# Performance work log

Hardware: AMD Instinct MI355X
Metric: run time of the kernel (lower is better)

The kernel has to match this reference:

```python
import jax, jax.numpy as jnp
import numpy as np

N, D = 65536, 1024  # points, in_dim == out_dim (required by the module's double use of linear.weight)


def setup_inputs() -> dict:
    key = jax.random.key(0)
    k_x, k_w, k_W, k_noise = jax.random.split(key, 4)
    x = jax.random.normal(k_x, (N, D), dtype=jnp.float32)
    w = jax.random.normal(k_w, (D,), dtype=jnp.float32)  # style vector (len == in_dim)
    # learned params of nn.Linear(in_dim, out_dim)
    W = jax.random.normal(k_W, (D, D), dtype=jnp.float32) * 0.02  # [out_dim, in_dim]
    b = jnp.zeros((D,), dtype=jnp.float32)
    # noise path: torch does randn(1, out_dim) * noise_strength each forward;
    # we materialize the raw noise deterministically for reproducibility.
    noise_strength = jnp.full((1,), 0.1, dtype=jnp.float32)
    noise_raw = jax.random.normal(k_noise, (1, D), dtype=jnp.float32)
    return {"x": x, "w": w, "W": W, "b": b,
            "noise_strength": noise_strength, "noise_raw": noise_raw}


def reference(x, w, W, b, noise_strength, noise_raw):
    # 1) plain linear: x1 = x @ W.T + b            [N, D]
    x1 = x @ W.T + b
    # 2) modulated_linear(x1, W, styles=w, noise, demodulate=True)
    #    demod coefficients: rsqrt(sum_j (W[o,j]*w[j])^2 + 1e-8)   [D]
    dcoefs = jax.lax.rsqrt(jnp.sum(jnp.square(W * w[None, :]), axis=1) + 1e-8)
    #    modulate input, dense matmul with raw weight
    x2 = (x1 * w) @ W.T                            # [N, D]
    #    fma: x2 * dcoefs + noise
    noise = noise_raw * noise_strength             # [1, D]
    x3 = x2 * dcoefs[None, :] + noise
    # 3) bias add + leaky_relu (torch default negative_slope=0.01)
    return jax.nn.leaky_relu(x3 + b, negative_slope=0.01)
```

## Files before the change

kernel.cpp:

```cpp
#include <hip/hip_runtime.h>
#include <hip/hip_bf16.h>

using bf16 = __hip_bfloat16;
typedef __attribute__((ext_vector_type(8))) short bf16x8;
typedef __attribute__((ext_vector_type(4))) float f32x4;

#define DDIM 1024

__device__ __forceinline__ void gload16(const bf16* g, bf16* l) {
    __builtin_amdgcn_global_load_lds(
        (const __attribute__((address_space(1))) void*)g,
        (__attribute__((address_space(3))) void*)l, 16, 0, 0);
}
__device__ __forceinline__ short f2b(float f) {
    return (short)__bfloat16_as_ushort(__float2bfloat16(f));
}


__global__ void prep_kernel(const float* __restrict__ W, const float* __restrict__ w,
                            const float* __restrict__ b, const float* __restrict__ nstr,
                            const float* __restrict__ nraw,
                            float* __restrict__ dco, float* __restrict__ add,
                            bf16* __restrict__ Qb) {
    int o = blockIdx.x;
    int lane = threadIdx.x;
    const float* Wrow = W + (size_t)o * DDIM;
    bf16* Qrow = Qb + (size_t)o * DDIM;
    float s = 0.f, c = 0.f;
    for (int j = lane; j < DDIM; j += 64) {
        float q = Wrow[j] * w[j];
        Qrow[j] = __float2bfloat16(q);
        s += q * q;
        c += b[j] * q;
    }
#pragma unroll
    for (int off = 32; off; off >>= 1) {
        s += __shfl_down(s, off);
        c += __shfl_down(c, off);
    }
    if (lane == 0) {
        float d = rsqrtf(s + 1e-8f);
        dco[o] = d;
        add[o] = c * d + nraw[o] * nstr[0] + b[o];
    }
}

__global__ void transpose_kernel(const float* __restrict__ W, bf16* __restrict__ Wt) {
    __shared__ bf16 tile[64][72];
    int bi = blockIdx.x * 64;
    int bj = blockIdx.y * 64;
    int r  = threadIdx.x >> 2;
    int c4 = (threadIdx.x & 3) * 16;
    const float* src = W + (size_t)(bi + r) * DDIM + bj + c4;
#pragma unroll
    for (int i = 0; i < 16; ++i) tile[r][c4 + i] = __float2bfloat16(src[i]);
    __syncthreads();
    bf16* dst = Wt + (size_t)(bj + r) * DDIM + bi + c4;
#pragma unroll
    for (int i = 0; i < 16; ++i) dst[i] = tile[c4 + i][r];
}

__global__ __launch_bounds__(256) void mgemm(const bf16* __restrict__ A,
                                             const bf16* __restrict__ B,
                                             bf16* __restrict__ C) {
    __shared__ bf16 lA[128 * 32];
    __shared__ bf16 lB[128 * 32];
    int tid  = threadIdx.x;
    int lane = tid & 63, wid = tid >> 6;
    int wr = wid >> 1, wc = wid & 1;
    int brow = blockIdx.x >> 3;
    int bcol = blockIdx.x & 7;
    const bf16* Ab = A + (size_t)brow * 128 * DDIM;
    const bf16* Bb = B + (size_t)bcol * 128 * DDIM;
    int srow = tid >> 2;
    int scol = (tid & 3) * 8;
    f32x4 acc[4][4];
#pragma unroll
    for (int m = 0; m < 4; ++m)
#pragma unroll
        for (int n = 0; n < 4; ++n) acc[m][n] = (f32x4){0.f, 0.f, 0.f, 0.f};
    int r16 = lane & 15, kh = lane >> 4;
    for (int k0 = 0; k0 < DDIM; k0 += 32) {
        gload16(Ab + (size_t)srow * DDIM + k0 + scol,        lA + tid * 8);
        gload16(Ab + (size_t)(srow + 64) * DDIM + k0 + scol, lA + (tid + 256) * 8);
        gload16(Bb + (size_t)srow * DDIM + k0 + scol,        lB + tid * 8);
        gload16(Bb + (size_t)(srow + 64) * DDIM + k0 + scol, lB + (tid + 256) * 8);
        __syncthreads();
        bf16x8 aF[4], bF[4];
#pragma unroll
        for (int m = 0; m < 4; ++m) {
            aF[m] = *(const bf16x8*)(lA + ((wr * 64 + m * 16 + r16) * 32 + kh * 8));
            bF[m] = *(const bf16x8*)(lB + ((wc * 64 + m * 16 + r16) * 32 + kh * 8));
        }
#pragma unroll
        for (int m = 0; m < 4; ++m)
#pragma unroll
            for (int n = 0; n < 4; ++n)
                acc[m][n] = __builtin_amdgcn_mfma_f32_16x16x32_bf16(aF[m], bF[n], acc[m][n], 0, 0, 0);
        __syncthreads();
    }
    int cb = lane & 15;
    int rb = (lane >> 4) * 4;
#pragma unroll
    for (int n = 0; n < 4; ++n) {
        int col = bcol * 128 + wc * 64 + n * 16 + cb;
#pragma unroll
        for (int m = 0; m < 4; ++m)
#pragma unroll
            for (int j = 0; j < 4; ++j) {
                int row = wr * 64 + m * 16 + rb + j;
                C[((size_t)brow * 128 + row) * DDIM + col] = __float2bfloat16(acc[m][n][j]);
            }
    }
}

#define BAR()  __builtin_amdgcn_s_barrier()
#define VMW(n) asm volatile("s_waitcnt vmcnt(" #n ")")
#define LGW()  asm volatile("s_waitcnt lgkmcnt(0)")

__global__ __launch_bounds__(512, 4) void big_gemm(
    const float* __restrict__ Af, const bf16* __restrict__ Bw,
    const float* __restrict__ dco, const float* __restrict__ add,
    float* __restrict__ Cf)
{
    __shared__ bf16 sA[2][256 * 32];
    __shared__ bf16 sB[2][128 * 32];

    const int tid  = threadIdx.x;
    const int lane = tid & 63;
    const int wid  = tid >> 6;
    const int wr   = wid >> 1, wc = wid & 1;
    const int r16  = lane & 15, kh = lane >> 4;
    const int fso  = (kh ^ ((r16 >> 1) & 3)) * 8;

    int bx  = blockIdx.x;
    int swz = (bx & 7) * 256 + (bx >> 3);
    int brow = swz >> 3, bcol = swz & 7;

    const float* Asrc_f = Af + (size_t)(brow * 256) * DDIM;
    const bf16*  Bsrc   = Bw + (size_t)(bcol * 128) * DDIM;

    const int sr  = tid >> 2;
    const int ssl = (tid & 3) ^ ((sr >> 1) & 3);

    f32x4 acc[4][4];
#pragma unroll
    for (int m = 0; m < 4; ++m)
#pragma unroll
        for (int n = 0; n < 4; ++n) acc[m][n] = (f32x4){0.f, 0.f, 0.f, 0.f};

    bf16x8 aF[4], bF[4];
    float4 gA0, gA1, gA2, gA3;

#define STAGE_B(buf, kt) do { \
    const bf16* _s = Bsrc + (size_t)sr * DDIM + ((kt) * 32 + ssl * 8); \
    gload16(_s, &sB[buf][tid * 8]); \
} while (0)

#define LOAD_A_F(kt) do { \
    const float* _p = Asrc_f + (size_t)sr * DDIM + ((kt) * 32 + (tid & 3) * 8); \
    gA0 = ((const float4*)_p)[0]; gA1 = ((const float4*)_p)[1]; \
    const float* _q = _p + 128 * DDIM; \
    gA2 = ((const float4*)_q)[0]; gA3 = ((const float4*)_q)[1]; \
} while (0)

#define WRITE_A(buf) do { \
    bf16x8 _pk; \
    _pk[0]=f2b(gA0.x); _pk[1]=f2b(gA0.y); _pk[2]=f2b(gA0.z); _pk[3]=f2b(gA0.w); \
    _pk[4]=f2b(gA1.x); _pk[5]=f2b(gA1.y); _pk[6]=f2b(gA1.z); _pk[7]=f2b(gA1.w); \
    *(bf16x8*)&sA[buf][sr * 32 + ssl * 8] = _pk; \
    _pk[0]=f2b(gA2.x); _pk[1]=f2b(gA2.y); _pk[2]=f2b(gA2.z); _pk[3]=f2b(gA2.w); \
    _pk[4]=f2b(gA3.x); _pk[5]=f2b(gA3.y); _pk[6]=f2b(gA3.z); _pk[7]=f2b(gA3.w); \
    *(bf16x8*)&sA[buf][(sr + 128) * 32 + ssl * 8] = _pk; \
} while (0)

#define RD_A(buf) do { \
    _Pragma("unroll") for (int _m = 0; _m < 4; ++_m) \
        aF[_m] = *(const bf16x8*)&sA[buf][(wr * 64 + _m * 16 + r16) * 32 + fso]; \
} while (0)

#define RD_B(buf) do { \
    _Pragma("unroll") for (int _n = 0; _n < 4; ++_n) \
        bF[_n] = *(const bf16x8*)&sB[buf][(wc * 64 + _n * 16 + r16) * 32 + fso]; \
} while (0)

#define MFMA16() do { \
    __builtin_amdgcn_s_setprio(1); \
    _Pragma("unroll") for (int _m = 0; _m < 4; ++_m) { \
        acc[_m][0] = __builtin_amdgcn_mfma_f32_16x16x32_bf16(aF[_m], bF[0], acc[_m][0], 0, 0, 0); \
        acc[_m][1] = __builtin_amdgcn_mfma_f32_16x16x32_bf16(aF[_m], bF[1], acc[_m][1], 0, 0, 0); \
        acc[_m][2] = __builtin_amdgcn_mfma_f32_16x16x32_bf16(aF[_m], bF[2], acc[_m][2], 0, 0, 0); \
        acc[_m][3] = __builtin_amdgcn_mfma_f32_16x16x32_bf16(aF[_m], bF[3], acc[_m][3], 0, 0, 0); \
    } \
    __builtin_amdgcn_s_setprio(0); \
} while (0)

    LOAD_A_F(0);
    STAGE_B(0, 0);
    VMW(1);
    WRITE_A(0);
    LOAD_A_F(1);
    LGW();
    VMW(4);
    BAR();

    for (int t = 0; t < 32; ++t) {
        int cur = t & 1, nxt = cur ^ 1;
        int t1 = t + 1; if (t1 > 31) t1 = 31;
        int t2 = t + 2; if (t2 > 31) t2 = 31;

        RD_A(cur); RD_B(cur);
        STAGE_B(nxt, t1);
        VMW(1);
        WRITE_A(nxt);
        LOAD_A_F(t2);
        LGW();
        BAR();
        MFMA16();
        VMW(4);
        BAR();
    }

    int cb = lane & 15;
    int rb = (lane >> 4) * 4;
#pragma unroll
    for (int n = 0; n < 4; ++n) {
        int col = bcol * 128 + wc * 64 + n * 16 + cb;
        float cm = dco[col], ca = add[col];
#pragma unroll
        for (int m = 0; m < 4; ++m) {
#pragma unroll
            for (int j = 0; j < 4; ++j) {
                int row = brow * 256 + wr * 64 + m * 16 + rb + j;
                float v = acc[m][n][j] * cm + ca;
                v = (v >= 0.f) ? v : 0.01f * v;
                Cf[(size_t)row * DDIM + col] = v;
            }
        }
    }
#undef STAGE_B
#undef LOAD_A_F
#undef WRITE_A
#undef RD_A
#undef RD_B
#undef MFMA16
}

extern "C" void kernel_launch(void* const* d_in, const int* in_sizes, int n_in,
                              void* d_out, int out_size, void* d_ws, size_t ws_size,
                              hipStream_t stream) {
    const float* x  = (const float*)d_in[0];
    const float* w  = (const float*)d_in[1];
    const float* W  = (const float*)d_in[2];
    const float* b  = (const float*)d_in[3];
    const float* ns = (const float*)d_in[4];
    const float* nr = (const float*)d_in[5];
    float* out = (float*)d_out;

    float* dco = (float*)d_ws;
    float* add = dco + DDIM;
    bf16*  Qb  = (bf16*)((char*)d_ws + 8192);
    bf16*  Wt  = (bf16*)((char*)d_ws + 8192 + 2097152);
    bf16*  Mt  = (bf16*)((char*)d_ws + 8192 + 2 * 2097152);

    int M = in_sizes[0] / DDIM;
    int grid = (M / 256) * (DDIM / 128);

    prep_kernel<<<DDIM, 64, 0, stream>>>(W, w, b, ns, nr, dco, add, Qb);
    transpose_kernel<<<dim3(16, 16), 256, 0, stream>>>(W, Wt);
    mgemm<<<64, 256, 0, stream>>>(Qb, Wt, Mt);
    big_gemm<<<grid, 512, 0, stream>>>(x, Mt, dco, add, out);
}
```

Before: 298.1 us.

## Load A fragments directly from global into registers, shrink block tile to 128x128

The big GEMM no longer stages the fp32 A operand through LDS. Each wave loads its own rows straight from global memory into registers and converts them to bf16 fragments, one k-step ahead. The block shrinks from 512 threads with a 256x128 tile to 256 threads with a 128x128 tile, so the grid doubles and each B tile is now fetched by twice as many blocks. The pipeline is reordered to prefetch B two stages ahead with one barrier per iteration, which removes the LDS writes and the second barrier but gives uncoalesced strided global A loads and more register pressure.

```diff
diff --git a/kernel.cpp b/kernel.cpp
--- a/kernel.cpp
+++ b/kernel.cpp
@@ -118,12 +118,11 @@
 #define VMW(n) asm volatile("s_waitcnt vmcnt(" #n ")")
 #define LGW()  asm volatile("s_waitcnt lgkmcnt(0)")
 
-__global__ __launch_bounds__(512, 4) void big_gemm(
+__global__ __launch_bounds__(256, 3) void big_gemm(
     const float* __restrict__ Af, const bf16* __restrict__ Bw,
     const float* __restrict__ dco, const float* __restrict__ add,
     float* __restrict__ Cf)
 {
-    __shared__ bf16 sA[2][256 * 32];
     __shared__ bf16 sB[2][128 * 32];
 
     const int tid  = threadIdx.x;
@@ -134,11 +133,11 @@
     const int fso  = (kh ^ ((r16 >> 1) & 3)) * 8;
 
     int bx  = blockIdx.x;
-    int swz = (bx & 7) * 256 + (bx >> 3);
+    int swz = (bx & 7) * 512 + (bx >> 3);
     int brow = swz >> 3, bcol = swz & 7;
 
-    const float* Asrc_f = Af + (size_t)(brow * 256) * DDIM;
-    const bf16*  Bsrc   = Bw + (size_t)(bcol * 128) * DDIM;
+    const float* Arow = Af + (size_t)(brow * 128 + wr * 64 + r16) * DDIM + kh * 8;
+    const bf16*  Bsrc = Bw + (size_t)(bcol * 128) * DDIM;
 
     const int sr  = tid >> 2;
     const int ssl = (tid & 3) ^ ((sr >> 1) & 3);
@@ -149,34 +148,30 @@
 #pragma unroll
         for (int n = 0; n < 4; ++n) acc[m][n] = (f32x4){0.f, 0.f, 0.f, 0.f};
 
+    float4 a0[4], a1[4];
     bf16x8 aF[4], bF[4];
-    float4 gA0, gA1, gA2, gA3;
+
+#define LOAD_A(kt) do { \
+    _Pragma("unroll") for (int _m = 0; _m < 4; ++_m) { \
+        const float* _p = Arow + (size_t)_m * 16 * DDIM + (kt) * 32; \
+        a0[_m] = ((const float4*)_p)[0]; \
+        a1[_m] = ((const float4*)_p)[1]; \
+    } \
+} while (0)
+
+#define CVT_A() do { \
+    _Pragma("unroll") for (int _m = 0; _m < 4; ++_m) { \
+        bf16x8 _pk; \
+        _pk[0]=f2b(a0[_m].x); _pk[1]=f2b(a0[_m].y); _pk[2]=f2b(a0[_m].z); _pk[3]=f2b(a0[_m].w); \
+        _pk[4]=f2b(a1[_m].x); _pk[5]=f2b(a1[_m].y); _pk[6]=f2b(a1[_m].z); _pk[7]=f2b(a1[_m].w); \
+        aF[_m] = _pk; \
+    } \
+} while (0)
 
 #define STAGE_B(buf, kt) do { \
-    const bf16* _s = Bsrc + (size_t)sr * DDIM + ((kt) * 32 + ssl * 8); \
-    gload16(_s, &sB[buf][tid * 8]); \
-} while (0)
-
-#define LOAD_A_F(kt) do { \
-    const float* _p = Asrc_f + (size_t)sr * DDIM + ((kt) * 32 + (tid & 3) * 8); \
-    gA0 = ((const float4*)_p)[0]; gA1 = ((const float4*)_p)[1]; \
-    const float* _q = _p + 128 * DDIM; \
-    gA2 = ((const float4*)_q)[0]; gA3 = ((const float4*)_q)[1]; \
-} while (0)
-
-#define WRITE_A(buf) do { \
-    bf16x8 _pk; \
-    _pk[0]=f2b(gA0.x); _pk[1]=f2b(gA0.y); _pk[2]=f2b(gA0.z); _pk[3]=f2b(gA0.w); \
-    _pk[4]=f2b(gA1.x); _pk[5]=f2b(gA1.y); _pk[6]=f2b(gA1.z); _pk[7]=f2b(gA1.w); \
-    *(bf16x8*)&sA[buf][sr * 32 + ssl * 8] = _pk; \
-    _pk[0]=f2b(gA2.x); _pk[1]=f2b(gA2.y); _pk[2]=f2b(gA2.z); _pk[3]=f2b(gA2.w); \
-    _pk[4]=f2b(gA3.x); _pk[5]=f2b(gA3.y); _pk[6]=f2b(gA3.z); _pk[7]=f2b(gA3.w); \
-    *(bf16x8*)&sA[buf][(sr + 128) * 32 + ssl * 8] = _pk; \
-} while (0)
-
-#define RD_A(buf) do { \
-    _Pragma("unroll") for (int _m = 0; _m < 4; ++_m) \
-        aF[_m] = *(const bf16x8*)&sA[buf][(wr * 64 + _m * 16 + r16) * 32 + fso]; \
+    const bf16* _s = Bsrc + (size_t)sr * DDIM + (kt) * 32 + ssl * 8; \
+    gload16(_s,              &sB[buf][tid * 8]); \
+    gload16(_s + 64 * DDIM,  &sB[buf][(tid + 256) * 8]); \
 } while (0)
 
 #define RD_B(buf) do { \
@@ -195,30 +190,25 @@
     __builtin_amdgcn_s_setprio(0); \
 } while (0)
 
-    LOAD_A_F(0);
     STAGE_B(0, 0);
-    VMW(1);
-    WRITE_A(0);
-    LOAD_A_F(1);
-    LGW();
-    VMW(4);
+    LOAD_A(0);
+    STAGE_B(1, 1);
+    VMW(2);
     BAR();
 
     for (int t = 0; t < 32; ++t) {
-        int cur = t & 1, nxt = cur ^ 1;
+        int cur = t & 1;
         int t1 = t + 1; if (t1 > 31) t1 = 31;
         int t2 = t + 2; if (t2 > 31) t2 = 31;
 
-        RD_A(cur); RD_B(cur);
-        STAGE_B(nxt, t1);
-        VMW(1);
-        WRITE_A(nxt);
-        LOAD_A_F(t2);
-        LGW();
+        CVT_A();
+        LOAD_A(t1);
+        RD_B(cur);
+        MFMA16();
+        VMW(8);
         BAR();
-        MFMA16();
-        VMW(4);
-        BAR();
+        STAGE_B(cur, t2);
+        VMW(2);
     }
 
     int cb = lane & 15;
@@ -231,17 +221,16 @@
         for (int m = 0; m < 4; ++m) {
 #pragma unroll
             for (int j = 0; j < 4; ++j) {
-                int row = brow * 256 + wr * 64 + m * 16 + rb + j;
+                int row = brow * 128 + wr * 64 + m * 16 + rb + j;
                 float v = acc[m][n][j] * cm + ca;
                 v = (v >= 0.f) ? v : 0.01f * v;
                 Cf[(size_t)row * DDIM + col] = v;
             }
         }
     }
+#undef LOAD_A
+#undef CVT_A
 #undef STAGE_B
-#undef LOAD_A_F
-#undef WRITE_A
-#undef RD_A
 #undef RD_B
 #undef MFMA16
 }
@@ -264,10 +253,10 @@
     bf16*  Mt  = (bf16*)((char*)d_ws + 8192 + 2 * 2097152);
 
     int M = in_sizes[0] / DDIM;
-    int grid = (M / 256) * (DDIM / 128);
+    int grid = (M / 128) * (DDIM / 128);
 
     prep_kernel<<<DDIM, 64, 0, stream>>>(W, w, b, ns, nr, dco, add, Qb);
     transpose_kernel<<<dim3(16, 16), 256, 0, stream>>>(W, Wt);
     mgemm<<<64, 256, 0, stream>>>(Qb, Wt, Mt);
-    big_gemm<<<grid, 512, 0, stream>>>(x, Mt, dco, add, out);
-}
+    big_gemm<<<grid, 256, 0, stream>>>(x, Mt, dco, add, out);
+}
```

Result: slower. 578.1 us (+93.9%).
